# Kernel optimization log

Measured on AMD Instinct MI355X. Metric: run time of the kernel, lower is better.

Reference implementation:

```python
import jax, jax.numpy as jnp
import numpy as np

T, B, S, D, H, E, F, K = 1024, 4, 1024, 1024, 16, 8, 2048, 2


def layer_norm(x, g, b, eps=1e-5):
    mu = x.mean(-1, keepdims=True)
    var = ((x - mu) ** 2).mean(-1, keepdims=True)
    return (x - mu) * jax.lax.rsqrt(var + eps) * g + b


def mha(q_in, k_in, v_in, Wq, bq, Wk, bk, Wv, bv, Wo, bo, n_heads, mask):
    # q_in: [Lq,B,D], k_in/v_in: [Lk,B,D]
    Lq, Bb, Dd = q_in.shape
    Lk = k_in.shape[0]
    hd = Dd // n_heads
    scale = 1.0 / np.sqrt(hd)
    q = ((q_in @ Wq + bq) * scale).reshape(Lq, Bb, n_heads, hd)
    k = (k_in @ Wk + bk).reshape(Lk, Bb, n_heads, hd)
    v = (v_in @ Wv + bv).reshape(Lk, Bb, n_heads, hd)
    scores = jnp.einsum('qbhd,kbhd->bhqk', q, k)  # [B,H,Lq,Lk]
    if mask is not None:
        scores = scores + mask  # additive mask broadcast over B,H
    p = jax.nn.softmax(scores, axis=-1)
    o = jnp.einsum('bhqk,kbhd->qbhd', p, v).reshape(Lq, Bb, Dd)
    return o @ Wo + bo


def moe_ffn(x2, gate_W, W1, b1, W2, b2, top_k):
    # x2: [N,D] flattened tokens. Top-k routing: softmax over the k selected logits.
    logits = x2 @ gate_W                      # [N,E]
    top_v, top_i = jax.lax.top_k(logits, top_k)
    gk = jax.nn.softmax(top_v, axis=-1)       # [N,k]
    gates = jnp.sum(jax.nn.one_hot(top_i, logits.shape[-1], dtype=x2.dtype) * gk[..., None], axis=1)  # [N,E] sparse
    out = jnp.zeros_like(x2)
    for e in range(W1.shape[0]):  # fixed small expert count
        h = jax.nn.relu(x2 @ W1[e] + b1[e])   # [N,F]
        out = out + gates[:, e:e + 1] * (h @ W2[e] + b2[e])
    return out


def _forward(x, encoder_out, self_attn_mask,
             ln1_g, ln1_b, ln2_g, ln2_b, ln3_g, ln3_b,
             sa_Wq, sa_bq, sa_Wk, sa_bk, sa_Wv, sa_bv, sa_Wo, sa_bo,
             ca_Wq, ca_bq, ca_Wk, ca_bk, ca_Wv, ca_bv, ca_Wo, ca_bo,
             gate_W, moe_W1, moe_b1, moe_W2, moe_b2):
    # pre-LN self-attention
    res = x
    xn = layer_norm(x, ln1_g, ln1_b)
    a = mha(xn, xn, xn, sa_Wq, sa_bq, sa_Wk, sa_bk, sa_Wv, sa_bv, sa_Wo, sa_bo, H, self_attn_mask)
    x = res + a
    # pre-LN cross-attention
    res = x
    xn = layer_norm(x, ln2_g, ln2_b)
    a = mha(xn, encoder_out, encoder_out, ca_Wq, ca_bq, ca_Wk, ca_bk, ca_Wv, ca_bv, ca_Wo, ca_bo, H, None)
    x = res + a
    # pre-LN MoE FFN
    res = x
    xn = layer_norm(x, ln3_g, ln3_b)
    m = moe_ffn(xn.reshape(-1, D), gate_W, moe_W1, moe_b1, moe_W2, moe_b2, K).reshape(x.shape)
    return res + m


def setup_inputs() -> dict:
    key = jax.random.key(0)
    ks = jax.random.split(key, 20)
    w = lambda k, shp: (jax.random.normal(k, shp, jnp.float32) * 0.02)
    causal = jnp.where(jnp.arange(T)[:, None] >= jnp.arange(T)[None, :], 0.0, -1e9).astype(jnp.float32)
    return {
        'x': jax.random.normal(ks[0], (T, B, D), jnp.float32),
        'encoder_out': jax.random.normal(ks[1], (S, B, D), jnp.float32),
        'self_attn_mask': causal,
        'ln1_g': jnp.ones((D,), jnp.float32), 'ln1_b': jnp.zeros((D,), jnp.float32),
        'ln2_g': jnp.ones((D,), jnp.float32), 'ln2_b': jnp.zeros((D,), jnp.float32),
        'ln3_g': jnp.ones((D,), jnp.float32), 'ln3_b': jnp.zeros((D,), jnp.float32),
        'sa_Wq': w(ks[2], (D, D)), 'sa_bq': jnp.zeros((D,), jnp.float32),
        'sa_Wk': w(ks[3], (D, D)), 'sa_bk': jnp.zeros((D,), jnp.float32),
        'sa_Wv': w(ks[4], (D, D)), 'sa_bv': jnp.zeros((D,), jnp.float32),
        'sa_Wo': w(ks[5], (D, D)), 'sa_bo': jnp.zeros((D,), jnp.float32),
        'ca_Wq': w(ks[6], (D, D)), 'ca_bq': jnp.zeros((D,), jnp.float32),
        'ca_Wk': w(ks[7], (D, D)), 'ca_bk': jnp.zeros((D,), jnp.float32),
        'ca_Wv': w(ks[8], (D, D)), 'ca_bv': jnp.zeros((D,), jnp.float32),
        'ca_Wo': w(ks[9], (D, D)), 'ca_bo': jnp.zeros((D,), jnp.float32),
        'gate_W': w(ks[10], (D, E)),
        'moe_W1': w(ks[11], (E, D, F)), 'moe_b1': jnp.zeros((E, F), jnp.float32),
        'moe_W2': w(ks[12], (E, F, D)), 'moe_b2': jnp.zeros((E, D), jnp.float32),
    }


def reference(x, encoder_out, self_attn_mask,
              ln1_g, ln1_b, ln2_g, ln2_b, ln3_g, ln3_b,
              sa_Wq, sa_bq, sa_Wk, sa_bk, sa_Wv, sa_bv, sa_Wo, sa_bo,
              ca_Wq, ca_bq, ca_Wk, ca_bk, ca_Wv, ca_bv, ca_Wo, ca_bo,
              gate_W, moe_W1, moe_b1, moe_W2, moe_b2):
    return _forward(x, encoder_out, self_attn_mask,
                    ln1_g, ln1_b, ln2_g, ln2_b, ln3_g, ln3_b,
                    sa_Wq, sa_bq, sa_Wk, sa_bk, sa_Wv, sa_bv, sa_Wo, sa_bo,
                    ca_Wq, ca_bq, ca_Wk, ca_bk, ca_Wv, ca_bv, ca_Wo, ca_bo,
                    gate_W, moe_W1, moe_b1, moe_W2, moe_b2)
```

## Files before the change

kernel.cpp:

```cpp
#include <hip/hip_runtime.h>
#include <hip/hip_bf16.h>

typedef unsigned short u16;
typedef float f32x4 __attribute__((ext_vector_type(4)));
typedef __bf16 bf16x8 __attribute__((ext_vector_type(8)));
typedef unsigned short u16x8 __attribute__((ext_vector_type(8)));
typedef unsigned short u16x4 __attribute__((ext_vector_type(4)));

__device__ __forceinline__ u16 f2bf(float f) {
    unsigned int u = __builtin_bit_cast(unsigned int, f);
    u += 0x7fffu + ((u >> 16) & 1u);
    return (u16)(u >> 16);
}
__device__ __forceinline__ float bf2f(u16 h) {
    unsigned int u = ((unsigned int)h) << 16;
    return __builtin_bit_cast(float, u);
}
__device__ __forceinline__ f32x4 mfma_bf16(u16x8 a, u16x8 b, f32x4 c) {
    return __builtin_amdgcn_mfma_f32_16x16x32_bf16(
        __builtin_bit_cast(bf16x8, a), __builtin_bit_cast(bf16x8, b), c, 0, 0, 0);
}
__device__ __forceinline__ void gload16(const void* g, void* l) {
    __builtin_amdgcn_global_load_lds(
        (const __attribute__((address_space(1))) unsigned int*)g,
        (__attribute__((address_space(3))) unsigned int*)l, 16, 0, 0);
}
__device__ __forceinline__ int swz_bid(int hw, int nwg) {
    return (hw & 7) * (nwg >> 3) + (hw >> 3);
}

template<bool GATHER>
__device__ __forceinline__ void gemm_core(
        const u16* __restrict__ Ab, const u16* __restrict__ Bb,
        int m0, int n0, int Klen, int Ksa, int Ksb, int cnt, const int* __restrict__ idx,
        u16* lds_a, u16* lds_b, f32x4 (&acc)[4][4]) {
    const int tid = threadIdx.x;
    const int w = tid >> 6, l = tid & 63;
    const int c8 = l & 7, r8 = l >> 3;
    const int lr = l & 15, lg = l >> 4;
    const int wr = (w >> 1) * 64, wc = (w & 1) * 64;
    const int swz = (c8 ^ r8) << 4;

    const char* asrc[4];
    const char* bsrc[4];
    #pragma unroll
    for (int i = 0; i < 4; i++) {
        int row = w * 32 + i * 8 + r8;
        int gr = m0 + row; if (gr > cnt - 1) gr = cnt - 1;
        if (GATHER) gr = idx[gr];
        asrc[i] = (const char*)Ab + (size_t)gr * Ksa * 2 + swz;
        bsrc[i] = (const char*)Bb + (size_t)(n0 + row) * Ksb * 2 + swz;
    }
    for (int k0 = 0; k0 < Klen; k0 += 64) {
        __syncthreads();
        #pragma unroll
        for (int i = 0; i < 4; i++) {
            gload16(asrc[i] + (size_t)k0 * 2, lds_a + (w * 32 + i * 8) * 64);
            gload16(bsrc[i] + (size_t)k0 * 2, lds_b + (w * 32 + i * 8) * 64);
        }
        __syncthreads();
        #pragma unroll
        for (int kk = 0; kk < 2; kk++) {
            u16x8 af[4], bfr[4];
            #pragma unroll
            for (int mi = 0; mi < 4; mi++) {
                int m = wr + mi * 16 + lr;
                af[mi] = *(const u16x8*)((const char*)lds_a + m * 128 + (((kk * 4 + lg) ^ (m & 7)) << 4));
            }
            #pragma unroll
            for (int ni = 0; ni < 4; ni++) {
                int n = wc + ni * 16 + lr;
                bfr[ni] = *(const u16x8*)((const char*)lds_b + n * 128 + (((kk * 4 + lg) ^ (n & 7)) << 4));
            }
            #pragma unroll
            for (int mi = 0; mi < 4; mi++)
                #pragma unroll
                for (int ni = 0; ni < 4; ni++)
                    acc[mi][ni] = mfma_bf16(af[mi], bfr[ni], acc[mi][ni]);
        }
    }
}

struct Slab5 { const u16* a; const u16* bt; const float* bias; u16* cb; float sc; };
struct Slabs5 { Slab5 s[5]; };

template<int MODE, int NSLAB>
__global__ __launch_bounds__(256, 3) void gemm_dense(
        Slabs5 P, const float* __restrict__ extra, float* __restrict__ Cf, int K) {
    __shared__ __align__(16) u16 lds_a[128 * 64];
    __shared__ __align__(16) u16 lds_b[128 * 64];
    const int gx = NSLAB * 8;
    const int lid = swz_bid((int)blockIdx.x + gx * (int)blockIdx.y, gx * 32);
    const int bx = lid % gx, by = lid / gx;
    const int slab = (NSLAB == 1) ? 0 : (bx >> 3);
    const int n0 = ((NSLAB == 1) ? bx : (bx & 7)) * 128;
    const int m0 = by * 128;
    f32x4 acc[4][4];
    #pragma unroll
    for (int i = 0; i < 4; i++)
        #pragma unroll
        for (int j = 0; j < 4; j++) acc[i][j] = (f32x4){0.f, 0.f, 0.f, 0.f};

    gemm_core<false>(P.s[slab].a, P.s[slab].bt, m0, n0, K, K, K, 0x7fffffff, nullptr, lds_a, lds_b, acc);

    const int tid = threadIdx.x, w = tid >> 6, l = tid & 63;
    const int lr = l & 15, lg = l >> 4, wr = (w >> 1) * 64, wc = (w & 1) * 64;
    const float* bias = P.s[slab].bias;
    #pragma unroll
    for (int ni = 0; ni < 4; ni++) {
        int col = n0 + wc + ni * 16 + lr;
        float bv = bias[col];
        #pragma unroll
        for (int mi = 0; mi < 4; mi++) {
            #pragma unroll
            for (int r = 0; r < 4; r++) {
                int row = m0 + wr + mi * 16 + lg * 4 + r;
                float v = acc[mi][ni][r] + bv;
                size_t off = (size_t)row * 1024 + col;
                if (MODE == 1) Cf[off] = v + extra[off];
                else           P.s[slab].cb[off] = f2bf(v * P.s[slab].sc);
            }
        }
    }
}

__global__ __launch_bounds__(256, 3) void gemm_moe1(
        const u16* __restrict__ XNb, const u16* __restrict__ W1b, const float* __restrict__ b1,
        u16* __restrict__ HB, const int* __restrict__ eidx,
        const int* __restrict__ ecnt, const int* __restrict__ eoff) {
    __shared__ __align__(16) u16 lds_a[128 * 64];
    __shared__ __align__(16) u16 lds_b[128 * 64];
    const int lid = swz_bid((int)blockIdx.x + 16 * ((int)blockIdx.y + 32 * (int)blockIdx.z), 4096);
    const int bx = lid & 15, rem = lid >> 4;
    const int by = rem & 31, e = rem >> 5;
    const int cnt = ecnt[e];
    const int m0 = by * 128;
    if (m0 >= cnt) return;
    const int n0 = bx * 128;
    const int* idx = eidx + e * 4096;
    f32x4 acc[4][4];
    #pragma unroll
    for (int i = 0; i < 4; i++)
        #pragma unroll
        for (int j = 0; j < 4; j++) acc[i][j] = (f32x4){0.f, 0.f, 0.f, 0.f};

    gemm_core<true>(XNb, W1b + (size_t)e * 2048 * 1024, m0, n0, 1024, 1024, 1024, cnt, idx, lds_a, lds_b, acc);

    const int tid = threadIdx.x, w = tid >> 6, l = tid & 63;
    const int lr = l & 15, lg = l >> 4, wr = (w >> 1) * 64, wc = (w & 1) * 64;
    u16* H = HB + (size_t)eoff[e] * 2048;
    const float* bias = b1 + (size_t)e * 2048;
    #pragma unroll
    for (int ni = 0; ni < 4; ni++) {
        int col = n0 + wc + ni * 16 + lr;
        float bv = bias[col];
        #pragma unroll
        for (int mi = 0; mi < 4; mi++) {
            #pragma unroll
            for (int r = 0; r < 4; r++) {
                int row = m0 + wr + mi * 16 + lg * 4 + r;
                if (row < cnt)
                    H[(size_t)row * 2048 + col] = f2bf(fmaxf(acc[mi][ni][r] + bv, 0.f));
            }
        }
    }
}

__global__ __launch_bounds__(256, 3) void gemm_moe2(
        const u16* __restrict__ HB, const u16* __restrict__ W2b, const float* __restrict__ b2,
        u16* __restrict__ Y,
        const int* __restrict__ ecnt, const int* __restrict__ eoff) {
    __shared__ __align__(16) u16 lds_a[128 * 64];
    __shared__ __align__(16) u16 lds_b[128 * 64];
    const int lid = swz_bid((int)blockIdx.x + 8 * ((int)blockIdx.y + 32 * (int)blockIdx.z), 2048);
    const int bx = lid & 7, rem = lid >> 3;
    const int by = rem & 31, e = rem >> 5;
    const int cnt = ecnt[e];
    const int m0 = by * 128;
    if (m0 >= cnt) return;
    const int n0 = bx * 128;
    const u16* Ae = HB + (size_t)eoff[e] * 2048;
    f32x4 acc[4][4];
    #pragma unroll
    for (int i = 0; i < 4; i++)
        #pragma unroll
        for (int j = 0; j < 4; j++) acc[i][j] = (f32x4){0.f, 0.f, 0.f, 0.f};

    gemm_core<false>(Ae, W2b + (size_t)e * 1024 * 2048, m0, n0, 2048, 2048, 2048, cnt, nullptr, lds_a, lds_b, acc);

    const int tid = threadIdx.x, w = tid >> 6, l = tid & 63;
    const int lr = l & 15, lg = l >> 4, wr = (w >> 1) * 64, wc = (w & 1) * 64;
    const float* bias = b2 + (size_t)e * 1024;
    u16* Ye = Y + (size_t)eoff[e] * 1024;
    #pragma unroll
    for (int ni = 0; ni < 4; ni++) {
        int col = n0 + wc + ni * 16 + lr;
        float bv = bias[col];
        #pragma unroll
        for (int mi = 0; mi < 4; mi++) {
            #pragma unroll
            for (int r = 0; r < 4; r++) {
                int row = m0 + wr + mi * 16 + lg * 4 + r;
                if (row < cnt)
                    Ye[(size_t)row * 1024 + col] = f2bf(acc[mi][ni][r] + bv);
            }
        }
    }
}

__global__ void combine_kernel(const float* __restrict__ g2, const int* __restrict__ slotmap,
                               const int* __restrict__ eoff, const u16* __restrict__ Y,
                               float* __restrict__ out) {
    int t = blockIdx.x * 4 + (threadIdx.x >> 6);
    int l = threadIdx.x & 63;
    int s0 = slotmap[t * 2], s1 = slotmap[t * 2 + 1];
    float g0 = g2[t * 2], g1 = g2[t * 2 + 1];
    int r0 = eoff[s0 >> 16] + (s0 & 0xffff);
    int r1 = eoff[s1 >> 16] + (s1 & 0xffff);
    const u16* y0 = Y + (size_t)r0 * 1024 + l * 16;
    const u16* y1 = Y + (size_t)r1 * 1024 + l * 16;
    float* op = out + (size_t)t * 1024 + l * 16;
    u16x8 a0 = *(const u16x8*)y0;
    u16x8 a1 = *(const u16x8*)(y0 + 8);
    u16x8 b0 = *(const u16x8*)y1;
    u16x8 b1 = *(const u16x8*)(y1 + 8);
    f32x4 o[4];
    #pragma unroll
    for (int j = 0; j < 4; j++) o[j] = *(const f32x4*)(op + j * 4);
    #pragma unroll
    for (int j = 0; j < 4; j++) {
        o[0][j] += g0 * bf2f(a0[j])     + g1 * bf2f(b0[j]);
        o[1][j] += g0 * bf2f(a0[j + 4]) + g1 * bf2f(b0[j + 4]);
        o[2][j] += g0 * bf2f(a1[j])     + g1 * bf2f(b1[j]);
        o[3][j] += g0 * bf2f(a1[j + 4]) + g1 * bf2f(b1[j + 4]);
    }
    #pragma unroll
    for (int j = 0; j < 4; j++) *(f32x4*)(op + j * 4) = o[j];
}

__global__ void ln_kernel(const float* __restrict__ X, const float* __restrict__ g,
                          const float* __restrict__ bt, u16* __restrict__ Yb) {
    int row = blockIdx.x * 4 + (threadIdx.x >> 6);
    int l = threadIdx.x & 63;
    const float* x = X + (size_t)row * 1024;
    f32x4 v[4];
    float s = 0.f, s2 = 0.f;
    #pragma unroll
    for (int i = 0; i < 4; i++) {
        v[i] = *reinterpret_cast<const f32x4*>(x + i * 256 + l * 4);
        #pragma unroll
        for (int j = 0; j < 4; j++) { s += v[i][j]; s2 += v[i][j] * v[i][j]; }
    }
    #pragma unroll
    for (int m = 1; m < 64; m <<= 1) { s += __shfl_xor(s, m); s2 += __shfl_xor(s2, m); }
    float mu = s * (1.f / 1024.f);
    float var = s2 * (1.f / 1024.f) - mu * mu;
    float rs = rsqrtf(var + 1e-5f);
    #pragma unroll
    for (int i = 0; i < 4; i++) {
        f32x4 gv = *reinterpret_cast<const f32x4*>(g + i * 256 + l * 4);
        f32x4 bv = *reinterpret_cast<const f32x4*>(bt + i * 256 + l * 4);
        u16x4 ob;
        #pragma unroll
        for (int j = 0; j < 4; j++) ob[j] = f2bf((v[i][j] - mu) * rs * gv[j] + bv[j]);
        *reinterpret_cast<u16x4*>(Yb + (size_t)row * 1024 + i * 256 + l * 4) = ob;
    }
}

__global__ void ln_gate_kernel(const float* __restrict__ X, const float* __restrict__ g,
                               const float* __restrict__ bt, u16* __restrict__ Yb,
                               const float* __restrict__ GW,
                               float* __restrict__ g2, int* __restrict__ top2) {
    int row = blockIdx.x * 4 + (threadIdx.x >> 6);
    int l = threadIdx.x & 63;
    const float* x = X + (size_t)row * 1024;
    f32x4 v[4];
    float s = 0.f, s2 = 0.f;
    #pragma unroll
    for (int i = 0; i < 4; i++) {
        v[i] = *reinterpret_cast<const f32x4*>(x + i * 256 + l * 4);
        #pragma unroll
        for (int j = 0; j < 4; j++) { s += v[i][j]; s2 += v[i][j] * v[i][j]; }
    }
    #pragma unroll
    for (int m = 1; m < 64; m <<= 1) { s += __shfl_xor(s, m); s2 += __shfl_xor(s2, m); }
    float mu = s * (1.f / 1024.f);
    float var = s2 * (1.f / 1024.f) - mu * mu;
    float rs = rsqrtf(var + 1e-5f);
    double p[8] = {0, 0, 0, 0, 0, 0, 0, 0};
    #pragma unroll
    for (int i = 0; i < 4; i++) {
        f32x4 gv = *reinterpret_cast<const f32x4*>(g + i * 256 + l * 4);
        f32x4 bv = *reinterpret_cast<const f32x4*>(bt + i * 256 + l * 4);
        u16x4 ob;
        #pragma unroll
        for (int j = 0; j < 4; j++) {
            float o = (v[i][j] - mu) * rs * gv[j] + bv[j];
            ob[j] = f2bf(o);
            const float* gw = GW + (size_t)(i * 256 + l * 4 + j) * 8;
            #pragma unroll
            for (int e = 0; e < 8; e++) p[e] += (double)o * (double)gw[e];
        }
        *reinterpret_cast<u16x4*>(Yb + (size_t)row * 1024 + i * 256 + l * 4) = ob;
    }
    #pragma unroll
    for (int e = 0; e < 8; e++) {
        #pragma unroll
        for (int m = 1; m < 64; m <<= 1) p[e] += __shfl_xor(p[e], m);
    }
    if (l == 0) {
        int i0 = 0; double v0 = p[0];
        #pragma unroll
        for (int e = 1; e < 8; e++) if (p[e] > v0) { v0 = p[e]; i0 = e; }
        int i1 = -1; double v1 = -1e300;
        #pragma unroll
        for (int e = 0; e < 8; e++) if (e != i0 && p[e] > v1) { v1 = p[e]; i1 = e; }
        float ex = __expf((float)(v1 - v0));
        float ga = 1.f / (1.f + ex);
        float gb = ex * ga;
        g2[row * 2] = ga; g2[row * 2 + 1] = gb;
        top2[row] = i0 | (i1 << 8);
    }
}

struct Ptr8 { const float* p[8]; };
__global__ void wtrans_kernel(Ptr8 srcs, u16* __restrict__ dst, int K, int N) {
    __shared__ float t[64][65];
    const float* W = srcs.p[blockIdx.z];
    u16* Wt = dst + (size_t)blockIdx.z * K * N;
    int k0 = blockIdx.y * 64, n0 = blockIdx.x * 64;
    int tx = threadIdx.x, ty = threadIdx.y;
    #pragma unroll
    for (int i = 0; i < 8; i++) t[ty + i * 8][tx] = W[(size_t)(k0 + ty + i * 8) * N + n0 + tx];
    __syncthreads();
    #pragma unroll
    for (int i = 0; i < 8; i++) Wt[(size_t)(n0 + ty + i * 8) * K + k0 + tx] = f2bf(t[tx][ty + i * 8]);
}

__global__ void cvt_kernel(const float* __restrict__ s, u16* __restrict__ d, int n) {
    int i = ((int)blockIdx.x * 256 + (int)threadIdx.x) * 8;
    if (i >= n) return;
    f32x4 a = *reinterpret_cast<const f32x4*>(s + i);
    f32x4 b = *reinterpret_cast<const f32x4*>(s + i + 4);
    u16x8 h;
    h[0] = f2bf(a[0]); h[1] = f2bf(a[1]); h[2] = f2bf(a[2]); h[3] = f2bf(a[3]);
    h[4] = f2bf(b[0]); h[5] = f2bf(b[1]); h[6] = f2bf(b[2]); h[7] = f2bf(b[3]);
    *reinterpret_cast<u16x8*>(d + i) = h;
}

__global__ void transpose_v(const u16* __restrict__ V, u16* __restrict__ Vt) {
    __shared__ u16 tile[32][34];
    int s0 = blockIdx.x * 32;
    int d0 = blockIdx.y * 32;
    int bh = blockIdx.z;
    int b = bh >> 4, h = bh & 15;
    int tx = threadIdx.x, ty = threadIdx.y;
    #pragma unroll
    for (int i = 0; i < 4; i++) {
        int s = s0 + ty + i * 8;
        tile[ty + i * 8][tx] = V[((size_t)s * 4 + b) * 1024 + h * 64 + d0 + tx];
    }
    __syncthreads();
    #pragma unroll
    for (int i = 0; i < 4; i++) {
        int d = d0 + ty + i * 8;
        Vt[((size_t)(bh * 64 + d)) * 1024 + s0 + tx] = tile[tx][ty + i * 8];
    }
}

template<bool CAUSAL>
__global__ __launch_bounds__(256, 4) void attn_kernel(
        const u16* __restrict__ Q, const u16* __restrict__ Km,
        const u16* __restrict__ Vt, u16* __restrict__ O) {
    __shared__ __align__(16) u16 kt_lds[64 * 64];
    __shared__ __align__(16) u16 vt_lds[64 * 64];
    __shared__ __align__(16) u16 p_lds[4][16 * 68];

    const int lid = swz_bid((int)blockIdx.x, 1024);
    const int qt = lid & 15;
    const int hh = (lid >> 4) & 15;
    const int b  = lid >> 8;
    const int tid = threadIdx.x;
    const int w = tid >> 6, l = tid & 63;
    const int lr = l & 15, lg = l >> 4;
    const int c8 = l & 7, r8 = l >> 3;
    const int qb = qt * 64;

    u16x8 qf0, qf1;
    {
        const u16* qp = Q + ((size_t)(qb + w * 16 + lr) * 4 + b) * 1024 + hh * 64 + lg * 8;
        qf0 = *(const u16x8*)qp;
        qf1 = *(const u16x8*)(qp + 32);
    }
    const u16* kbase = Km + (size_t)b * 1024 + (size_t)hh * 64 + ((c8 ^ r8) << 3);
    const u16* vbase = Vt + ((size_t)(b * 16 + hh) * 64) * 1024 + ((c8 ^ r8) << 3);

    f32x4 o[4];
    #pragma unroll
    for (int ni = 0; ni < 4; ni++) o[ni] = (f32x4){0.f, 0.f, 0.f, 0.f};
    float Mr[4], Lr[4];
    #pragma unroll
    for (int r = 0; r < 4; r++) { Mr[r] = -1e30f; Lr[r] = 0.f; }

    const int nkt = CAUSAL ? (qt + 1) : 16;

    for (int kt = 0; kt < nkt; ++kt) {
        __syncthreads();
        #pragma unroll
        for (int i = 0; i < 2; i++) {
            int rrow = w * 16 + i * 8 + r8;
            gload16(kbase + (size_t)(kt * 64 + rrow) * 4096, &kt_lds[(w * 16 + i * 8) * 64]);
            gload16(vbase + (size_t)rrow * 1024 + kt * 64, &vt_lds[(w * 16 + i * 8) * 64]);
        }
        __syncthreads();

        f32x4 s4[4];
        __builtin_amdgcn_s_setprio(1);
        #pragma unroll
        for (int g = 0; g < 4; g++) {
            int krow = g * 16 + lr;
            const char* kl = (const char*)kt_lds + krow * 128;
            u16x8 kf0 = *(const u16x8*)(kl + ((lg ^ (krow & 7)) << 4));
            u16x8 kf1 = *(const u16x8*)(kl + (((lg + 4) ^ (krow & 7)) << 4));
            s4[g] = mfma_bf16(qf0, kf0, (f32x4){0.f, 0.f, 0.f, 0.f});
            s4[g] = mfma_bf16(qf1, kf1, s4[g]);
        }
        __builtin_amdgcn_s_setprio(0);
        if (CAUSAL && kt == qt) {
            #pragma unroll
            for (int g = 0; g < 4; g++) {
                int kg = kt * 64 + g * 16 + lr;
                #pragma unroll
                for (int r = 0; r < 4; r++) {
                    int qg = qb + w * 16 + lg * 4 + r;
                    if (kg > qg) s4[g][r] = -1e30f;
                }
            }
        }
        float mx[4];
        #pragma unroll
        for (int r = 0; r < 4; r++) {
            float m_ = fmaxf(fmaxf(s4[0][r], s4[1][r]), fmaxf(s4[2][r], s4[3][r]));
            m_ = fmaxf(m_, __shfl_xor(m_, 1));
            m_ = fmaxf(m_, __shfl_xor(m_, 2));
            m_ = fmaxf(m_, __shfl_xor(m_, 4));
            m_ = fmaxf(m_, __shfl_xor(m_, 8));
            mx[r] = m_;
        }
        bool fast = __all((mx[0] <= Mr[0] + 8.f) && (mx[1] <= Mr[1] + 8.f) &&
                          (mx[2] <= Mr[2] + 8.f) && (mx[3] <= Mr[3] + 8.f));
        #pragma unroll
        for (int r = 0; r < 4; r++) {
            if (!fast) {
                float newM = fmaxf(Mr[r], mx[r]);
                float corr = __expf(Mr[r] - newM);
                Lr[r] *= corr;
                o[0][r] *= corr; o[1][r] *= corr; o[2][r] *= corr; o[3][r] *= corr;
                Mr[r] = newM;
            }
            float p0 = __expf(s4[0][r] - Mr[r]);
            float p1 = __expf(s4[1][r] - Mr[r]);
            float p2 = __expf(s4[2][r] - Mr[r]);
            float p3 = __expf(s4[3][r] - Mr[r]);
            float ps = (p0 + p1) + (p2 + p3);
            ps += __shfl_xor(ps, 1); ps += __shfl_xor(ps, 2);
            ps += __shfl_xor(ps, 4); ps += __shfl_xor(ps, 8);
            Lr[r] += ps;
            int prow = lg * 4 + r;
            p_lds[w][prow * 68 + lr] = f2bf(p0);
            p_lds[w][prow * 68 + 16 + lr] = f2bf(p1);
            p_lds[w][prow * 68 + 32 + lr] = f2bf(p2);
            p_lds[w][prow * 68 + 48 + lr] = f2bf(p3);
        }
        asm volatile("s_waitcnt lgkmcnt(0)" ::: "memory");
        __builtin_amdgcn_s_setprio(1);
        #pragma unroll
        for (int kk = 0; kk < 2; kk++) {
            u16x8 pf = *(const u16x8*)&p_lds[w][lr * 68 + kk * 32 + lg * 8];
            #pragma unroll
            for (int ni = 0; ni < 4; ni++) {
                int vrow = ni * 16 + lr;
                const char* vl = (const char*)vt_lds + vrow * 128;
                u16x8 vf = *(const u16x8*)(vl + (((kk * 4 + lg) ^ (vrow & 7)) << 4));
                o[ni] = mfma_bf16(pf, vf, o[ni]);
            }
        }
        __builtin_amdgcn_s_setprio(0);
    }
    #pragma unroll
    for (int ni = 0; ni < 4; ni++) {
        #pragma unroll
        for (int r = 0; r < 4; r++) {
            int row = qb + w * 16 + lg * 4 + r;
            int col = ni * 16 + lr;
            O[((size_t)row * 4 + b) * 1024 + hh * 64 + col] = f2bf(o[ni][r] / Lr[r]);
        }
    }
}

__global__ void build_lists(const int* __restrict__ top2, int* __restrict__ eidx,
                            int* __restrict__ ecnt, int* __restrict__ slotmap) {
    const int e = blockIdx.x;
    const int tid = threadIdx.x;
    const int w = tid >> 6, l = tid & 63;
    __shared__ int wcnt[4];
    int base = 0;
    for (int c = 0; c < 4096; c += 256) {
        int tok = c + tid;
        int t2 = top2[tok];
        bool pf = ((t2 & 0xff) == e);
        bool ps = (((t2 >> 8) & 0xff) == e);
        bool pred = pf || ps;
        unsigned long long mask = __ballot(pred);
        if (l == 0) wcnt[w] = __popcll(mask);
        __syncthreads();
        int wb = base;
        for (int i = 0; i < w; i++) wb += wcnt[i];
        int pos = __popcll(mask & ((1ull << l) - 1ull));
        if (pred) {
            eidx[e * 4096 + wb + pos] = tok;
            slotmap[tok * 2 + (pf ? 0 : 1)] = (e << 16) | (wb + pos);
        }
        base += wcnt[0] + wcnt[1] + wcnt[2] + wcnt[3];
        __syncthreads();
    }
    if (tid == 0) ecnt[e] = base;
}

__global__ void scan_kernel(const int* __restrict__ ecnt, int* __restrict__ eoff) {
    if (threadIdx.x == 0) {
        int s = 0;
        for (int e = 0; e < 8; e++) { eoff[e] = s; s += ecnt[e]; }
    }
}

extern "C" void kernel_launch(void* const* d_in, const int* in_sizes, int n_in,
                              void* d_out, int out_size, void* d_ws, size_t ws_size,
                              hipStream_t stream) {
    const float* x    = (const float*)d_in[0];
    const float* enc  = (const float*)d_in[1];
    const float* ln1g = (const float*)d_in[3];
    const float* ln1b = (const float*)d_in[4];
    const float* ln2g = (const float*)d_in[5];
    const float* ln2b = (const float*)d_in[6];
    const float* ln3g = (const float*)d_in[7];
    const float* ln3b = (const float*)d_in[8];
    const float* saWq = (const float*)d_in[9];  const float* sabq = (const float*)d_in[10];
    const float* saWk = (const float*)d_in[11]; const float* sabk = (const float*)d_in[12];
    const float* saWv = (const float*)d_in[13]; const float* sabv = (const float*)d_in[14];
    const float* saWo = (const float*)d_in[15]; const float* sabo = (const float*)d_in[16];
    const float* caWq = (const float*)d_in[17]; const float* cabq = (const float*)d_in[18];
    const float* caWk = (const float*)d_in[19]; const float* cabk = (const float*)d_in[20];
    const float* caWv = (const float*)d_in[21]; const float* cabv = (const float*)d_in[22];
    const float* caWo = (const float*)d_in[23]; const float* cabo = (const float*)d_in[24];
    const float* gateW = (const float*)d_in[25];
    const float* W1 = (const float*)d_in[26]; const float* b1 = (const float*)d_in[27];
    const float* W2 = (const float*)d_in[28]; const float* b2 = (const float*)d_in[29];
    float* out = (float*)d_out;
    char* W = (char*)d_ws;

    const size_t MB = 1ull << 20;
    u16*   Wattn = (u16*)(W);
    u16*   Qb    = (u16*)(W + 16 * MB);
    u16*   Kb    = (u16*)(W + 24 * MB);
    u16*   Vb    = (u16*)(W + 32 * MB);
    u16*   VTb   = (u16*)(W + 40 * MB);
    u16*   ATb   = (u16*)(W + 48 * MB);
    u16*   encb  = (u16*)(W + 56 * MB);
    u16*   XNb   = (u16*)(W + 64 * MB);
    float* X1    = (float*)(W + 72 * MB);
    u16*   K2b   = (u16*)(W + 88 * MB);
    u16*   V2b   = (u16*)(W + 96 * MB);
    u16*   HB    = (u16*)(W + 88 * MB);
    u16*   W1b   = (u16*)(W);
    u16*   W2b   = (u16*)(W + 32 * MB);
    u16*   Yc    = (u16*)(W);
    float* g2    = (float*)(W + 120 * MB);
    int*   eidx  = (int*)(W + 120 * MB + 128 * 1024);
    int*   ecnt  = (int*)(W + 120 * MB + 256 * 1024);
    int*   eoff  = ecnt + 16;
    int*   top2  = (int*)(W + 120 * MB + 272 * 1024);
    int*   slotmap = (int*)(W + 120 * MB + 320 * 1024);

    dim3 bw(64, 8);
    const float SC = 0.125f;

    {
        Ptr8 p; p.p[0]=saWq; p.p[1]=saWk; p.p[2]=saWv; p.p[3]=saWo;
                p.p[4]=caWq; p.p[5]=caWk; p.p[6]=caWv; p.p[7]=caWo;
        wtrans_kernel<<<dim3(16, 16, 8), bw, 0, stream>>>(p, Wattn, 1024, 1024);
    }
    cvt_kernel<<<2048, 256, 0, stream>>>(enc, encb, 4096 * 1024);

    ln_kernel<<<1024, 256, 0, stream>>>(x, ln1g, ln1b, XNb);
    {
        Slabs5 P;
        P.s[0] = {XNb,  Wattn,               sabq, Qb,  SC };
        P.s[1] = {XNb,  Wattn + 1 * 1048576, sabk, Kb,  1.f};
        P.s[2] = {XNb,  Wattn + 2 * 1048576, sabv, Vb,  1.f};
        P.s[3] = {encb, Wattn + 5 * 1048576, cabk, K2b, 1.f};
        P.s[4] = {encb, Wattn + 6 * 1048576, cabv, V2b, 1.f};
        gemm_dense<2, 5><<<dim3(40, 32), 256, 0, stream>>>(P, nullptr, nullptr, 1024);
    }
    transpose_v<<<dim3(32, 2, 64), dim3(32, 8), 0, stream>>>(Vb, VTb);
    attn_kernel<true><<<1024, 256, 0, stream>>>(Qb, Kb, VTb, ATb);
    {
        Slabs5 P; P.s[0] = {ATb, Wattn + 3 * 1048576, sabo, nullptr, 1.f};
        gemm_dense<1, 1><<<dim3(8, 32), 256, 0, stream>>>(P, x, X1, 1024);
    }

    ln_kernel<<<1024, 256, 0, stream>>>(X1, ln2g, ln2b, XNb);
    {
        Slabs5 P; P.s[0] = {XNb, Wattn + 4 * 1048576, cabq, Qb, SC};
        gemm_dense<2, 1><<<dim3(8, 32), 256, 0, stream>>>(P, nullptr, nullptr, 1024);
    }
    transpose_v<<<dim3(32, 2, 64), dim3(32, 8), 0, stream>>>(V2b, VTb);
    attn_kernel<false><<<1024, 256, 0, stream>>>(Qb, K2b, VTb, ATb);
    {
        Slabs5 P; P.s[0] = {ATb, Wattn + 7 * 1048576, cabo, nullptr, 1.f};
        gemm_dense<1, 1><<<dim3(8, 32), 256, 0, stream>>>(P, X1, out, 1024);
    }

    {
        Ptr8 p1; for (int e = 0; e < 8; e++) p1.p[e] = W1 + (size_t)e * 1024 * 2048;
        wtrans_kernel<<<dim3(32, 16, 8), bw, 0, stream>>>(p1, W1b, 1024, 2048);
        Ptr8 p2; for (int e = 0; e < 8; e++) p2.p[e] = W2 + (size_t)e * 2048 * 1024;
        wtrans_kernel<<<dim3(16, 32, 8), bw, 0, stream>>>(p2, W2b, 2048, 1024);
    }
    ln_gate_kernel<<<1024, 256, 0, stream>>>(out, ln3g, ln3b, XNb, gateW, g2, top2);
    build_lists<<<8, 256, 0, stream>>>(top2, eidx, ecnt, slotmap);
    scan_kernel<<<1, 64, 0, stream>>>(ecnt, eoff);
    gemm_moe1<<<dim3(16, 32, 8), 256, 0, stream>>>(XNb, W1b, b1, HB, eidx, ecnt, eoff);
    gemm_moe2<<<dim3(8, 32, 8), 256, 0, stream>>>(HB, W2b, b2, Yc, ecnt, eoff);
    combine_kernel<<<1024, 256, 0, stream>>>(g2, slotmap, eoff, Yc, out);
}
```

Before: 497.9 us.

## Double-buffer LDS tiles in MoE expert GEMMs to overlap loads with MFMA

Adds a pipelined GEMM core that keeps two LDS stages per operand and issues the global-to-LDS loads for tile t+2 while tile t is computed, using vmcnt waits and barriers. Both MoE expert GEMM kernels switch to it, with LDS buffers doubled and launch bounds lowered from 3 to 2 blocks per CU. The aim is to hide global load latency behind matrix work. The cost is more LDS per block and lower occupancy.

```diff
diff --git a/kernel.cpp b/kernel.cpp
--- a/kernel.cpp
+++ b/kernel.cpp
@@ -77,6 +77,78 @@
                 #pragma unroll
                 for (int ni = 0; ni < 4; ni++)
                     acc[mi][ni] = mfma_bf16(af[mi], bfr[ni], acc[mi][ni]);
+        }
+    }
+}
+
+template<bool GATHER>
+__device__ __forceinline__ void gemm_core_pipe(
+        const u16* __restrict__ Ab, const u16* __restrict__ Bb,
+        int m0, int n0, int Klen, int Ksa, int Ksb, int cnt, const int* __restrict__ idx,
+        u16* lds_a, u16* lds_b, f32x4 (&acc)[4][4]) {
+    const int tid = threadIdx.x;
+    const int w = tid >> 6, l = tid & 63;
+    const int c8 = l & 7, r8 = l >> 3;
+    const int lr = l & 15, lg = l >> 4;
+    const int wr = (w >> 1) * 64, wc = (w & 1) * 64;
+    const int swz = (c8 ^ r8) << 4;
+
+    const char* asrc[4];
+    const char* bsrc[4];
+    #pragma unroll
+    for (int i = 0; i < 4; i++) {
+        int row = w * 32 + i * 8 + r8;
+        int gr = m0 + row; if (gr > cnt - 1) gr = cnt - 1;
+        if (GATHER) gr = idx[gr];
+        asrc[i] = (const char*)Ab + (size_t)gr * Ksa * 2 + swz;
+        bsrc[i] = (const char*)Bb + (size_t)(n0 + row) * Ksb * 2 + swz;
+    }
+    const int nt = Klen >> 6;
+    #pragma unroll
+    for (int i = 0; i < 4; i++) {
+        gload16(asrc[i], lds_a + (w * 32 + i * 8) * 64);
+        gload16(bsrc[i], lds_b + (w * 32 + i * 8) * 64);
+    }
+    if (1 < nt) {
+        #pragma unroll
+        for (int i = 0; i < 4; i++) {
+            gload16(asrc[i] + 128, lds_a + 8192 + (w * 32 + i * 8) * 64);
+            gload16(bsrc[i] + 128, lds_b + 8192 + (w * 32 + i * 8) * 64);
+        }
+    }
+    for (int t = 0; t < nt; t++) {
+        if (t + 1 < nt) asm volatile("s_waitcnt vmcnt(8)" ::: "memory");
+        else            asm volatile("s_waitcnt vmcnt(0)" ::: "memory");
+        __builtin_amdgcn_s_barrier();
+        const u16* la = lds_a + (t & 1) * 8192;
+        const u16* lb = lds_b + (t & 1) * 8192;
+        #pragma unroll
+        for (int kk = 0; kk < 2; kk++) {
+            u16x8 af[4], bfr[4];
+            #pragma unroll
+            for (int mi = 0; mi < 4; mi++) {
+                int m = wr + mi * 16 + lr;
+                af[mi] = *(const u16x8*)((const char*)la + m * 128 + (((kk * 4 + lg) ^ (m & 7)) << 4));
+            }
+            #pragma unroll
+            for (int ni = 0; ni < 4; ni++) {
+                int n = wc + ni * 16 + lr;
+                bfr[ni] = *(const u16x8*)((const char*)lb + n * 128 + (((kk * 4 + lg) ^ (n & 7)) << 4));
+            }
+            #pragma unroll
+            for (int mi = 0; mi < 4; mi++)
+                #pragma unroll
+                for (int ni = 0; ni < 4; ni++)
+                    acc[mi][ni] = mfma_bf16(af[mi], bfr[ni], acc[mi][ni]);
+        }
+        asm volatile("s_waitcnt lgkmcnt(0)" ::: "memory");
+        __builtin_amdgcn_s_barrier();
+        if (t + 2 < nt) {
+            #pragma unroll
+            for (int i = 0; i < 4; i++) {
+                gload16(asrc[i] + (size_t)(t + 2) * 128, lds_a + (t & 1) * 8192 + (w * 32 + i * 8) * 64);
+                gload16(bsrc[i] + (size_t)(t + 2) * 128, lds_b + (t & 1) * 8192 + (w * 32 + i * 8) * 64);
+            }
         }
     }
 }
@@ -124,12 +196,12 @@
     }
 }
 
-__global__ __launch_bounds__(256, 3) void gemm_moe1(
+__global__ __launch_bounds__(256, 2) void gemm_moe1(
         const u16* __restrict__ XNb, const u16* __restrict__ W1b, const float* __restrict__ b1,
         u16* __restrict__ HB, const int* __restrict__ eidx,
         const int* __restrict__ ecnt, const int* __restrict__ eoff) {
-    __shared__ __align__(16) u16 lds_a[128 * 64];
-    __shared__ __align__(16) u16 lds_b[128 * 64];
+    __shared__ __align__(16) u16 lds_a[2 * 128 * 64];
+    __shared__ __align__(16) u16 lds_b[2 * 128 * 64];
     const int lid = swz_bid((int)blockIdx.x + 16 * ((int)blockIdx.y + 32 * (int)blockIdx.z), 4096);
     const int bx = lid & 15, rem = lid >> 4;
     const int by = rem & 31, e = rem >> 5;
@@ -144,7 +216,7 @@
         #pragma unroll
         for (int j = 0; j < 4; j++) acc[i][j] = (f32x4){0.f, 0.f, 0.f, 0.f};
 
-    gemm_core<true>(XNb, W1b + (size_t)e * 2048 * 1024, m0, n0, 1024, 1024, 1024, cnt, idx, lds_a, lds_b, acc);
+    gemm_core_pipe<true>(XNb, W1b + (size_t)e * 2048 * 1024, m0, n0, 1024, 1024, 1024, cnt, idx, lds_a, lds_b, acc);
 
     const int tid = threadIdx.x, w = tid >> 6, l = tid & 63;
     const int lr = l & 15, lg = l >> 4, wr = (w >> 1) * 64, wc = (w & 1) * 64;
@@ -166,12 +238,12 @@
     }
 }
 
-__global__ __launch_bounds__(256, 3) void gemm_moe2(
+__global__ __launch_bounds__(256, 2) void gemm_moe2(
         const u16* __restrict__ HB, const u16* __restrict__ W2b, const float* __restrict__ b2,
         u16* __restrict__ Y,
         const int* __restrict__ ecnt, const int* __restrict__ eoff) {
-    __shared__ __align__(16) u16 lds_a[128 * 64];
-    __shared__ __align__(16) u16 lds_b[128 * 64];
+    __shared__ __align__(16) u16 lds_a[2 * 128 * 64];
+    __shared__ __align__(16) u16 lds_b[2 * 128 * 64];
     const int lid = swz_bid((int)blockIdx.x + 8 * ((int)blockIdx.y + 32 * (int)blockIdx.z), 2048);
     const int bx = lid & 7, rem = lid >> 3;
     const int by = rem & 31, e = rem >> 5;
@@ -186,7 +258,7 @@
         #pragma unroll
         for (int j = 0; j < 4; j++) acc[i][j] = (f32x4){0.f, 0.f, 0.f, 0.f};
 
-    gemm_core<false>(Ae, W2b + (size_t)e * 1024 * 2048, m0, n0, 2048, 2048, 2048, cnt, nullptr, lds_a, lds_b, acc);
+    gemm_core_pipe<false>(Ae, W2b + (size_t)e * 1024 * 2048, m0, n0, 2048, 2048, 2048, cnt, nullptr, lds_a, lds_b, acc);
 
     const int tid = threadIdx.x, w = tid >> 6, l = tid & 63;
     const int lr = l & 15, lg = l >> 4, wr = (w >> 1) * 64, wc = (w & 1) * 64;
```

Result: slower. 523.2 us (+5.1%).
